# Kernel optimization log

Hardware: AMD Instinct MI355X
Metric: run time of the kernel (lower is better)

The kernel has to match this reference:

```python
import jax, jax.numpy as jnp
import numpy as np

N_NODES = 2000
LN_EPS = 1e-5
NEG_SLOPE = 0.2  # PyG GATConv default


def _gat(xg, W, b, a_src, a_dst, src, dst):
    # xg: [G, N, Fin]; single-head GATConv, add_self_loops=False
    h = xg @ W                      # [G, N, H]
    es = h @ a_src                  # [G, N]
    ed = h @ a_dst                  # [G, N]
    e = jax.nn.leaky_relu(es[:, src] + ed[:, dst], NEG_SLOPE)  # [G, E]

    def seg_softmax(e_g):
        m = jax.ops.segment_max(e_g, dst, num_segments=N_NODES)
        ex = jnp.exp(e_g - m[dst])
        s = jax.ops.segment_sum(ex, dst, num_segments=N_NODES)
        return ex / (s[dst] + 1e-16)

    alpha = jax.vmap(seg_softmax)(e)            # [G, E]
    msg = alpha[..., None] * h[:, src]          # [G, E, H]
    agg = jax.vmap(lambda m_: jax.ops.segment_sum(m_, dst, num_segments=N_NODES))(msg)
    return agg + b                              # [G, N, H]


def _gcn_layer(x, W, b, a_src, a_dst, src, dst):
    # x: [B, N, T, F] -- faithfully replicate original permute + raw reshape
    B, N, T, F = x.shape
    x_in = jnp.transpose(x, (0, 2, 1, 3)).reshape(B * T, N, F)
    out = _gat(x_in, W, b, a_src, a_dst, src, dst)          # [B*T, N, H]
    out = jax.nn.gelu(out.reshape(B, T, N, -1), approximate=False)
    # original does .reshape(B, N, T, -1) on a [B,T,N,H]-contiguous tensor
    return out.reshape(B, N, T, -1)


def _lstm(x, Wih, Whh, bih, bhh):
    # x: [BN, T, Fin]; torch LSTM gate order i,f,g,o
    BN, T, _ = x.shape
    H = Whh.shape[1]
    xz = x @ Wih.T + (bih + bhh)                # [BN, T, 4H]

    def step(carry, z_t):
        h, c = carry
        z = z_t + h @ Whh.T
        i, f, g, o = jnp.split(z, 4, axis=-1)
        c = jax.nn.sigmoid(f) * c + jax.nn.sigmoid(i) * jnp.tanh(g)
        h = jax.nn.sigmoid(o) * jnp.tanh(c)
        return (h, c), h

    init = (jnp.zeros((BN, H), x.dtype), jnp.zeros((BN, H), x.dtype))
    _, hs = jax.lax.scan(step, init, jnp.swapaxes(xz, 0, 1))
    return jnp.swapaxes(hs, 0, 1)               # [BN, T, H]


def setup_inputs() -> dict:
    key = jax.random.key(0)
    ks = jax.random.split(key, 20)
    B, N, T, NX, H, PL, NY, E = 2, N_NODES, 24, 8, 64, 12, 1, 32000
    p = {}
    p["x"] = jax.random.normal(ks[0], (B, N, T, NX), jnp.float32)
    p["edge_src"] = jax.random.randint(ks[1], (E,), 0, N, jnp.int32)
    p["edge_dst"] = jax.random.randint(ks[2], (E,), 0, N, jnp.int32)
    p["fc_W"] = jax.random.normal(ks[3], (NX, H), jnp.float32) / np.sqrt(NX)
    p["fc_b"] = jnp.zeros((H,), jnp.float32)
    for i, tag in enumerate(["g1", "g2"]):
        p[f"{tag}_W"] = jax.random.normal(ks[4 + 4 * i], (H, H), jnp.float32) / np.sqrt(H)
        p[f"{tag}_b"] = jnp.zeros((H,), jnp.float32)
        p[f"{tag}_asrc"] = jax.random.normal(ks[5 + 4 * i], (H,), jnp.float32) / np.sqrt(H)
        p[f"{tag}_adst"] = jax.random.normal(ks[6 + 4 * i], (H,), jnp.float32) / np.sqrt(H)
    p["lstm_Wih"] = jax.random.normal(ks[12], (4 * H, H), jnp.float32) / np.sqrt(H)
    p["lstm_Whh"] = jax.random.normal(ks[13], (4 * H, H), jnp.float32) / np.sqrt(H)
    p["lstm_bih"] = jnp.zeros((4 * H,), jnp.float32)
    p["lstm_bhh"] = jnp.zeros((4 * H,), jnp.float32)
    p["ln_g"] = jnp.ones((H,), jnp.float32)
    p["ln_b"] = jnp.zeros((H,), jnp.float32)
    p["dense_W"] = jax.random.normal(ks[14], (H, PL * NY), jnp.float32) / np.sqrt(H)
    p["dense_b"] = jnp.zeros((PL * NY,), jnp.float32)
    return p


def reference(x, edge_src, edge_dst, fc_W, fc_b,
              g1_W, g1_b, g1_asrc, g1_adst,
              g2_W, g2_b, g2_asrc, g2_adst,
              lstm_Wih, lstm_Whh, lstm_bih, lstm_bhh,
              ln_g, ln_b, dense_W, dense_b):
    B, N, T, _ = x.shape
    PRED_LEN, NY = 12, 1
    x_h = x @ fc_W + fc_b                                        # [B,N,T,H]
    g1 = _gcn_layer(x_h, g1_W, g1_b, g1_asrc, g1_adst, edge_src, edge_dst)
    g2 = _gcn_layer(g1, g2_W, g2_b, g2_asrc, g2_adst, edge_src, edge_dst)
    H = g2.shape[-1]
    lout = _lstm(g2.reshape(B * N, T, -1), lstm_Wih, lstm_Whh, lstm_bih, lstm_bhh)
    lout = lout.reshape(B, N, T, H)
    mu = jnp.mean(lout, axis=-1, keepdims=True)
    var = jnp.mean(jnp.square(lout - mu), axis=-1, keepdims=True)
    h = (lout - mu) / jnp.sqrt(var + LN_EPS) * ln_g + ln_b
    out = h[:, :, -1:, :] @ dense_W + dense_b                    # [B,N,1,PL*NY]
    return out.reshape(B, N, PRED_LEN, NY)
```

## Files before the change

kernel.cpp:

```cpp
#include <hip/hip_runtime.h>
#include <hip/hip_bf16.h>
#include <math.h>

#define B_   2
#define N_   2000
#define T_   24
#define NX_  8
#define H_   64
#define G_   (B_*T_)
#define E_   32000
#define BN_  (B_*N_)
#define TH_  (T_*H_)
#define NTH_ (N_*T_*H_)
#define GNH_ (G_*N_*H_)
#define NPARAM_ 43340
#define NPARAM_PAD_ 43392
#define XSTRIDE 1568
#define HPAD 96
#define DEGCAP 64

using bf16 = __hip_bfloat16;
typedef short bf16x8 __attribute__((ext_vector_type(8)));
typedef float f32x4  __attribute__((ext_vector_type(4)));

__device__ __forceinline__ float uasf(unsigned u){ return __uint_as_float(u); }
__device__ __forceinline__ float wave_sum(float v){
  #pragma unroll
  for (int o = 32; o > 0; o >>= 1) v += __shfl_xor(v, o, 64);
  return v;
}
__device__ __forceinline__ float fastrcp(float x){ return __builtin_amdgcn_rcpf(x); }
__device__ __forceinline__ float sigf(float x){ return fastrcp(1.f + __expf(-x)); }
__device__ __forceinline__ float tanhfast(float x){ return 1.f - 2.f*fastrcp(1.f + __expf(2.f*x)); }
__device__ __forceinline__ float gelu_fast(float x){
  float s = x*0.70710678118654752f;
  float a = fabsf(s);
  float t = fastrcp(1.f + 0.3275911f*a);
  float p = t*(0.254829592f + t*(-0.284496736f + t*(1.421413741f + t*(-1.453152027f + t*1.061405429f))));
  float er = 1.f - p*__expf(-a*a);
  er = (s < 0.f) ? -er : er;
  return 0.5f*x*(1.f + er);
}
__device__ __forceinline__ unsigned f2bf_rtn(float f){
  unsigned u = __float_as_uint(f);
  u += 0x7fffu + ((u >> 16) & 1u);
  return u >> 16;
}
__device__ __forceinline__ bf16x8 pack8(float4 a, float4 b){
  bf16x8 v;
  v[0]=(short)f2bf_rtn(a.x); v[1]=(short)f2bf_rtn(a.y);
  v[2]=(short)f2bf_rtn(a.z); v[3]=(short)f2bf_rtn(a.w);
  v[4]=(short)f2bf_rtn(b.x); v[5]=(short)f2bf_rtn(b.y);
  v[6]=(short)f2bf_rtn(b.z); v[7]=(short)f2bf_rtn(b.w);
  return v;
}

struct ConvArgs {
  const void* src[18];
  int off[19];
};
__global__ __launch_bounds__(256) void prep_kernel(
    ConvArgs a, const unsigned* __restrict__ xw,
    float* __restrict__ dst, int* __restrict__ flag,
    int* __restrict__ cnt_g,
    float* __restrict__ wc, float* __restrict__ bc){
  __shared__ int scnt;
  int tid = threadIdx.x;
  if (tid == 0) scnt = 0;
  __syncthreads();
  int c = 0;
  for (int i = tid; i < 4096; i += 256){
    unsigned e = (xw[i] >> 7) & 0xffu;
    if (e >= 100u && e <= 140u) c++;
  }
  atomicAdd(&scnt, c);
  __syncthreads();
  int isbf = (scnt > 3276) ? 1 : 0;
  int bid = blockIdx.x;

  if (bid < 170){
    if (bid == 0 && tid == 0) *flag = isbf;
    int i = bid*256 + tid;
    if (i < NPARAM_){
      int seg = 0;
      while (i >= a.off[seg+1]) seg++;
      int j = i - a.off[seg];
      float v;
      if (isbf) v = uasf(((unsigned)((const unsigned short*)a.src[seg])[j]) << 16);
      else      v = ((const float*)a.src[seg])[j];
      dst[i] = v;
    }
  } else if (bid == 170){
    for (int i = tid; i < N_; i += 256) cnt_g[i] = 0;
  } else if (bid < 180){
    int lane = tid & 63, wave = tid >> 6;
    int b = bid - 171;
    const unsigned short* fcWu = (const unsigned short*)a.src[0];
    const unsigned short* fcbu = (const unsigned short*)a.src[1];
    const unsigned short* g1Wu = (const unsigned short*)a.src[2];
    const float* fcWf = (const float*)a.src[0];
    const float* fcbf = (const float*)a.src[1];
    const float* g1Wf = (const float*)a.src[2];
    #pragma unroll
    for (int s = 0; s < 16; ++s){
      int o = b*64 + wave*16 + s;
      int r = o >> 6;
      int n = o & 63;
      float fa, fb;
      if (isbf){
        fa = (r < 8) ? uasf(((unsigned)fcWu[r*64 + lane]) << 16)
                     : uasf(((unsigned)fcbu[lane]) << 16);
        fb = uasf(((unsigned)g1Wu[lane*64 + n]) << 16);
      } else {
        fa = (r < 8) ? fcWf[r*64 + lane] : fcbf[lane];
        fb = g1Wf[lane*64 + n];
      }
      float sv = wave_sum(fa * fb);
      if (lane == 0){
        if (r < 8) wc[r*64 + n] = sv;
        else       bc[n] = sv;
      }
    }
  } else {
    int lane = tid & 63, wave = tid >> 6;
    int isA = (bid == 180);
    const unsigned short* g2Wu = (const unsigned short*)a.src[6];
    const float* g2Wf = (const float*)a.src[6];
    const unsigned short* au = (const unsigned short*)a.src[isA ? 8 : 9];
    const float* af = (const float*)a.src[isA ? 8 : 9];
    float fb = isbf ? uasf(((unsigned)au[lane]) << 16) : af[lane];
    #pragma unroll
    for (int s = 0; s < 16; ++s){
      int k = wave*16 + s;
      float fa = isbf ? uasf(((unsigned)g2Wu[k*64 + lane]) << 16)
                      : uasf(f2bf_rtn(g2Wf[k*64 + lane]) << 16);
      float sv = wave_sum(fa * fb);
      if (lane == 0) wc[(isA ? 576 : 640) + k] = sv;
    }
  }
}

__global__ __launch_bounds__(256) void gat_h1_fused_kernel(
    const void* __restrict__ xraw, const int* __restrict__ flag,
    const int* __restrict__ esrc, const int* __restrict__ edst,
    int* __restrict__ cnt_g, int* __restrict__ slot,
    const float* __restrict__ wc, const float* __restrict__ bc,
    const float* __restrict__ asrc, const float* __restrict__ adst,
    unsigned short* __restrict__ hbuf, float* __restrict__ es, float* __restrict__ ed){
  if (blockIdx.x < 125){
    int e = blockIdx.x*256 + threadIdx.x;
    int d = edst[e];
    int pos = atomicAdd(&cnt_g[d], 1);
    if (pos < DEGCAP) slot[(d << 6) + pos] = esrc[e];
  }
  int lane = threadIdx.x & 63, wave = threadIdx.x >> 6;
  int q = lane >> 4, c = lane & 15;
  int isbf = *flag;
  bf16x8 Bf[4];
  #pragma unroll
  for (int nt = 0; nt < 4; ++nt){
    bf16x8 v;
    #pragma unroll
    for (int j = 0; j < 8; ++j)
      v[j] = (q == 0) ? (short)f2bf_rtn(wc[j*64 + nt*16 + c]) : (short)0;
    Bf[nt] = v;
  }
  float bcv[4];
  #pragma unroll
  for (int nt = 0; nt < 4; ++nt) bcv[nt] = bc[nt*16 + c];
  float aS[4], aD[4];
  #pragma unroll
  for (int nt = 0; nt < 4; ++nt){ aS[nt] = asrc[nt*16+c]; aD[nt] = adst[nt*16+c]; }

  int w = blockIdx.x*4 + wave;
  #pragma unroll
  for (int it = 0; it < 2; ++it){
    int tile = w*2 + it;
    int p0 = tile*16;
    int g  = p0 / N_, n0 = p0 - g*N_;
    int bb = g / T_,  tt = g - bb*T_;
    bf16x8 A0;
    #pragma unroll
    for (int j = 0; j < 8; ++j) A0[j] = 0;
    if (q == 0){
      size_t rowelt = ((size_t)(bb*N_ + n0 + c)*T_ + tt)*NX_;
      if (isbf){
        A0 = *(const bf16x8*)((const unsigned short*)xraw + rowelt);
      } else {
        const float4* xr4 = (const float4*)((const float*)xraw + rowelt);
        A0 = pack8(xr4[0], xr4[1]);
      }
    }
    f32x4 acc[4];
    #pragma unroll
    for (int nt = 0; nt < 4; ++nt){ acc[nt][0]=bcv[nt]; acc[nt][1]=bcv[nt]; acc[nt][2]=bcv[nt]; acc[nt][3]=bcv[nt]; }
    #pragma unroll
    for (int nt = 0; nt < 4; ++nt) acc[nt] = __builtin_amdgcn_mfma_f32_16x16x32_bf16(A0, Bf[nt], acc[nt], 0, 0, 0);

    #pragma unroll
    for (int nt = 0; nt < 4; ++nt){
      #pragma unroll
      for (int r = 0; r < 4; ++r)
        hbuf[(size_t)(p0 + q*4 + r)*H_ + nt*16 + c] = (unsigned short)f2bf_rtn(acc[nt][r]);
    }
    #pragma unroll
    for (int r = 0; r < 4; ++r){
      float e1 = acc[0][r]*aS[0] + acc[1][r]*aS[1] + acc[2][r]*aS[2] + acc[3][r]*aS[3];
      float e2 = acc[0][r]*aD[0] + acc[1][r]*aD[1] + acc[2][r]*aD[2] + acc[3][r]*aD[3];
      #pragma unroll
      for (int o = 8; o > 0; o >>= 1){
        e1 += __shfl_xor(e1, o, 64);
        e2 += __shfl_xor(e2, o, 64);
      }
      if (c == 0){
        es[p0 + q*4 + r] = e1;
        ed[p0 + q*4 + r] = e2;
      }
    }
  }
}

__global__ __launch_bounds__(256) void gat_agg1_kernel(
    const unsigned short* __restrict__ hbuf, const float* __restrict__ es, const float* __restrict__ ed,
    const int* __restrict__ cnt_g, const int* __restrict__ slot,
    const float* __restrict__ bias, unsigned short* __restrict__ goutb,
    const float* __restrict__ wa2, const float* __restrict__ wd2,
    float* __restrict__ es2, float* __restrict__ ed2){
  int lane = threadIdx.x & 63, wave = threadIdx.x >> 6;
  int qd = lane >> 4, ln = lane & 15;
  int gd = (blockIdx.x*4 + wave)*4 + qd;
  int g = gd / N_, d = gd - g*N_;
  int start = d << 6;
  int deg = min(cnt_g[d], DEGCAP);
  const float* esg = es + (size_t)g*N_;
  float edv = ed[(size_t)g*N_ + d];
  const char* hg = (const char*)(hbuf + (size_t)g*N_*H_);
  unsigned lanoff = ((unsigned)ln) << 3;
  int hbase = qd << 4;
  int dm = deg;
  dm = max(dm, __shfl_xor(dm, 16, 64));
  dm = max(dm, __shfl_xor(dm, 32, 64));
  int NC = (dm + 15) >> 4;

  int svk[4];
  #pragma unroll
  for (int k = 0; k < 4; ++k) svk[k] = 0;
  #pragma unroll
  for (int k = 0; k < 4; ++k){
    int i = k*16 + ln;
    if (k < NC && i < deg) svk[k] = slot[start + i];
  }
  float exk[4]; float ssum = 0.f;
  #pragma unroll
  for (int k = 0; k < 4; ++k){
    int i = k*16 + ln;
    float e = 0.f;
    if (k < NC && i < deg){
      float v = esg[svk[k]] + edv;
      v = v > 0.f ? v : 0.2f*v;
      e = __expf(fminf(v, 60.f));
    }
    exk[k] = e; ssum += e;
  }
  #pragma unroll
  for (int o = 8; o > 0; o >>= 1) ssum += __shfl_xor(ssum, o, 64);
  float inv = fastrcp(ssum + 1e-16f);
  unsigned pwk[4];
  #pragma unroll
  for (int k = 0; k < 4; ++k)
    pwk[k] = (f2bf_rtn(exk[k]*inv) << 16) | (unsigned)svk[k];

  float a0 = 0.f, a1 = 0.f, a2 = 0.f, a3 = 0.f;
  for (int k = 0; k < NC; ++k){
    unsigned pw = pwk[k];
    int myrem = deg - k*16;
    int remw = dm - k*16; if (remw > 16) remw = 16;
    for (int j0 = 0; j0 < remw; j0 += 8){
      unsigned wv[8]; float aa[8]; unsigned off[8];
      #pragma unroll
      for (int u = 0; u < 8; ++u){
        int j = j0 + u;
        wv[u] = (unsigned)__shfl((int)pw, hbase + j, 64);
        aa[u] = (j < myrem) ? uasf(wv[u] & 0xffff0000u) : 0.f;
        off[u] = ((wv[u] & 0xffffu) << 7) + lanoff;
      }
      uint2 hv[8];
      #pragma unroll
      for (int u = 0; u < 8; ++u)
        hv[u] = *(const uint2*)(hg + off[u]);
      #pragma unroll
      for (int u = 0; u < 8; ++u){
        a0 = fmaf(aa[u], uasf(hv[u].x << 16), a0);
        a1 = fmaf(aa[u], uasf(hv[u].x & 0xffff0000u), a1);
        a2 = fmaf(aa[u], uasf(hv[u].y << 16), a2);
        a3 = fmaf(aa[u], uasf(hv[u].y & 0xffff0000u), a3);
      }
    }
  }
  float4 bv = ((const float4*)bias)[ln];
  float g0 = gelu_fast(a0 + bv.x), g1 = gelu_fast(a1 + bv.y);
  float g2v = gelu_fast(a2 + bv.z), g3 = gelu_fast(a3 + bv.w);
  uint2 ov;
  ov.x = f2bf_rtn(g0) | (f2bf_rtn(g1) << 16);
  ov.y = f2bf_rtn(g2v) | (f2bf_rtn(g3) << 16);
  ((uint2*)(goutb + (size_t)gd*H_))[ln] = ov;

  float h0 = uasf(ov.x << 16), h1v = uasf(ov.x & 0xffff0000u);
  float h2v = uasf(ov.y << 16), h3v = uasf(ov.y & 0xffff0000u);
  f32x4 wa = *(const f32x4*)(wa2 + ln*4);
  f32x4 wd = *(const f32x4*)(wd2 + ln*4);
  float e1 = h0*wa[0] + h1v*wa[1] + h2v*wa[2] + h3v*wa[3];
  float e2 = h0*wd[0] + h1v*wd[1] + h2v*wd[2] + h3v*wd[3];
  #pragma unroll
  for (int o = 8; o > 0; o >>= 1){
    e1 += __shfl_xor(e1, o, 64);
    e2 += __shfl_xor(e2, o, 64);
  }
  if (ln == 0){
    int bbp = gd / (N_*T_);
    int rem = gd - bbp*(N_*T_);
    int np  = rem / T_;
    int tp  = rem - np*T_;
    int pprime = (bbp*T_ + tp)*N_ + np;
    es2[pprime] = e1;
    ed2[pprime] = e2;
  }
}

__global__ __launch_bounds__(256) void gat_agg2_kernel(
    const unsigned short* __restrict__ goutb, const float* __restrict__ es, const float* __restrict__ ed,
    const int* __restrict__ cnt_g, const int* __restrict__ slot,
    const float* __restrict__ W, const float* __restrict__ b2,
    unsigned short* __restrict__ outb){
  __shared__ __align__(16) float vlds[4*256];
  int lane = threadIdx.x & 63, wave = threadIdx.x >> 6;
  int qd = lane >> 4, ln = lane & 15;
  int gd = (blockIdx.x*4 + wave)*4 + qd;
  int g = gd / N_, d = gd - g*N_;
  int bb2 = g / T_, t2 = g - bb2*T_;
  int start = d << 6;
  int deg = min(cnt_g[d], DEGCAP);
  const float* esg = es + (size_t)g*N_;
  float edv = ed[(size_t)g*N_ + d];
  const char* hgb = (const char*)goutb + (size_t)bb2*(size_t)(NTH_*2) + (size_t)t2*128 + (((unsigned)ln) << 3);
  int hbase = qd << 4;
  int dm = deg;
  dm = max(dm, __shfl_xor(dm, 16, 64));
  dm = max(dm, __shfl_xor(dm, 32, 64));
  int NC = (dm + 15) >> 4;

  bf16x8 Bf[4][2];
  #pragma unroll
  for (int nt = 0; nt < 4; ++nt){
    #pragma unroll
    for (int ks = 0; ks < 2; ++ks){
      bf16x8 v;
      #pragma unroll
      for (int j = 0; j < 8; ++j)
        v[j] = (short)f2bf_rtn(W[(ks*32 + qd*8 + j)*H_ + nt*16 + ln]);
      Bf[nt][ks] = v;
    }
  }
  float bcv[4];
  #pragma unroll
  for (int nt = 0; nt < 4; ++nt) bcv[nt] = b2[nt*16 + ln];

  int svk[4];
  #pragma unroll
  for (int k = 0; k < 4; ++k) svk[k] = 0;
  #pragma unroll
  for (int k = 0; k < 4; ++k){
    int i = k*16 + ln;
    if (k < NC && i < deg) svk[k] = slot[start + i];
  }
  float exk[4]; float ssum = 0.f;
  #pragma unroll
  for (int k = 0; k < 4; ++k){
    int i = k*16 + ln;
    float e = 0.f;
    if (k < NC && i < deg){
      float v = esg[svk[k]] + edv;
      v = v > 0.f ? v : 0.2f*v;
      e = __expf(fminf(v, 60.f));
    }
    exk[k] = e; ssum += e;
  }
  #pragma unroll
  for (int o = 8; o > 0; o >>= 1) ssum += __shfl_xor(ssum, o, 64);
  float inv = fastrcp(ssum + 1e-16f);
  unsigned pwk[4];
  #pragma unroll
  for (int k = 0; k < 4; ++k)
    pwk[k] = (f2bf_rtn(exk[k]*inv) << 16) | (unsigned)svk[k];

  float a0 = 0.f, a1 = 0.f, a2 = 0.f, a3 = 0.f;
  for (int k = 0; k < NC; ++k){
    unsigned pw = pwk[k];
    int myrem = deg - k*16;
    int remw = dm - k*16; if (remw > 16) remw = 16;
    for (int j0 = 0; j0 < remw; j0 += 8){
      unsigned wv[8]; float aa[8]; unsigned off[8];
      #pragma unroll
      for (int u = 0; u < 8; ++u){
        int j = j0 + u;
        wv[u] = (unsigned)__shfl((int)pw, hbase + j, 64);
        aa[u] = (j < myrem) ? uasf(wv[u] & 0xffff0000u) : 0.f;
        off[u] = (wv[u] & 0xffffu) * 3072u;
      }
      uint2 hv[8];
      #pragma unroll
      for (int u = 0; u < 8; ++u)
        hv[u] = *(const uint2*)(hgb + off[u]);
      #pragma unroll
      for (int u = 0; u < 8; ++u){
        a0 = fmaf(aa[u], uasf(hv[u].x << 16), a0);
        a1 = fmaf(aa[u], uasf(hv[u].x & 0xffff0000u), a1);
        a2 = fmaf(aa[u], uasf(hv[u].y << 16), a2);
        a3 = fmaf(aa[u], uasf(hv[u].y & 0xffff0000u), a3);
      }
    }
  }

  unsigned short* vu = (unsigned short*)vlds + wave*512;
  uint2 vp;
  vp.x = f2bf_rtn(a0) | (f2bf_rtn(a1) << 16);
  vp.y = f2bf_rtn(a2) | (f2bf_rtn(a3) << 16);
  *(uint2*)(vu + qd*64 + ln*4) = vp;
  bf16x8 Af0 = *(const bf16x8*)(vu + (ln & 3)*64 + qd*8);
  bf16x8 Af1 = *(const bf16x8*)(vu + (ln & 3)*64 + 32 + qd*8);

  f32x4 acc[4];
  #pragma unroll
  for (int nt = 0; nt < 4; ++nt){ acc[nt][0]=0.f; acc[nt][1]=0.f; acc[nt][2]=0.f; acc[nt][3]=0.f; }
  #pragma unroll
  for (int nt = 0; nt < 4; ++nt) acc[nt] = __builtin_amdgcn_mfma_f32_16x16x32_bf16(Af0, Bf[nt][0], acc[nt], 0, 0, 0);
  #pragma unroll
  for (int nt = 0; nt < 4; ++nt) acc[nt] = __builtin_amdgcn_mfma_f32_16x16x32_bf16(Af1, Bf[nt][1], acc[nt], 0, 0, 0);

  float* vf = vlds + wave*256;
  if (qd == 0){
    #pragma unroll
    for (int nt = 0; nt < 4; ++nt){
      #pragma unroll
      for (int r = 0; r < 4; ++r)
        vf[r*64 + nt*16 + ln] = acc[nt][r] + bcv[nt];
    }
  }
  __syncthreads();
  f32x4 vo = *(const f32x4*)(vf + qd*64 + ln*4);
  uint2 ov;
  ov.x = f2bf_rtn(gelu_fast(vo[0])) | (f2bf_rtn(gelu_fast(vo[1])) << 16);
  ov.y = f2bf_rtn(gelu_fast(vo[2])) | (f2bf_rtn(gelu_fast(vo[3])) << 16);
  ((uint2*)(outb + (size_t)gd*H_))[ln] = ov;
}

__global__ __launch_bounds__(256) void lstm_final_kernel(
    const unsigned short* __restrict__ xinb,
    const float* __restrict__ Wih,
    const float* __restrict__ Whh,
    const float* __restrict__ bih, const float* __restrict__ bhh,
    const float* __restrict__ lng, const float* __restrict__ lnb,
    const float* __restrict__ dW, const float* __restrict__ db,
    const int* __restrict__ flag, void* __restrict__ outv){
  __shared__ __align__(16) unsigned short Xlds[4*XSTRIDE];
  __shared__ __align__(16) unsigned short Hlds[2][4*HPAD];
  __shared__ float smH[4][68];
  int tid = threadIdx.x;
  int lane = tid & 63, wave = tid >> 6;
  int q = lane >> 4, c = lane & 15;
  int cc = c >> 2;
  int s0 = blockIdx.x * 4;

  {
    const unsigned short* xg = xinb + (size_t)s0 * TH_;
    #pragma unroll
    for (int ch0 = 0; ch0 < 12; ch0 += 4){
      int ch = ch0 + wave;
      int r = ch / 3, jj = ch - r*3;
      bf16x8 v = *(const bf16x8*)(xg + r*1536 + jj*512 + lane*8);
      *(bf16x8*)(Xlds + r*XSTRIDE + jj*512 + lane*8) = v;
    }
  }

  bf16x8 Bf[4][4];
  #pragma unroll
  for (int g = 0; g < 4; ++g){
    int n = g*64 + wave*16 + c;
    #pragma unroll
    for (int ks = 0; ks < 4; ++ks){
      const float* srcp = (ks < 2) ? (Whh + (size_t)n*64 + ks*32 + q*8)
                                   : (Wih + (size_t)n*64 + (ks-2)*32 + q*8);
      float4 a = ((const float4*)srcp)[0];
      float4 b = ((const float4*)srcp)[1];
      Bf[g][ks] = pack8(a, b);
    }
  }
  float bsum[4];
  #pragma unroll
  for (int g = 0; g < 4; ++g){
    int n = g*64 + wave*16 + c;
    bsum[g] = bih[n] + bhh[n];
  }
  for (int i = tid; i < 4*HPAD; i += 256) Hlds[0][i] = 0;
  float cst = 0.f;
  __syncthreads();

  const unsigned short* xrow = Xlds + cc*XSTRIDE;
  bf16x8 Ax0 = *(const bf16x8*)(xrow + q*8);
  bf16x8 Ax1 = *(const bf16x8*)(xrow + 32 + q*8);

  int buf = 0;
  for (int t = 0; t < T_; ++t){
    bf16x8 Ah0 = *(const bf16x8*)(Hlds[buf] + cc*HPAD + q*8);
    bf16x8 Ah1 = *(const bf16x8*)(Hlds[buf] + cc*HPAD + 32 + q*8);

    f32x4 acc[4];
    #pragma unroll
    for (int g = 0; g < 4; ++g){ acc[g][0]=bsum[g]; acc[g][1]=bsum[g]; acc[g][2]=bsum[g]; acc[g][3]=bsum[g]; }
    #pragma unroll
    for (int g = 0; g < 4; ++g) acc[g] = __builtin_amdgcn_mfma_f32_16x16x32_bf16(Ax0, Bf[g][2], acc[g], 0, 0, 0);
    #pragma unroll
    for (int g = 0; g < 4; ++g) acc[g] = __builtin_amdgcn_mfma_f32_16x16x32_bf16(Ax1, Bf[g][3], acc[g], 0, 0, 0);
    #pragma unroll
    for (int g = 0; g < 4; ++g) acc[g] = __builtin_amdgcn_mfma_f32_16x16x32_bf16(Ah0, Bf[g][0], acc[g], 0, 0, 0);
    #pragma unroll
    for (int g = 0; g < 4; ++g) acc[g] = __builtin_amdgcn_mfma_f32_16x16x32_bf16(Ah1, Bf[g][1], acc[g], 0, 0, 0);

    int tn = (t < T_-1) ? t+1 : T_-1;
    bf16x8 AxN0 = *(const bf16x8*)(xrow + tn*64 + q*8);
    bf16x8 AxN1 = *(const bf16x8*)(xrow + tn*64 + 32 + q*8);

    float zi = acc[0][0], zf = acc[1][0], zg = acc[2][0], zo = acc[3][0];
    cst = sigf(zf)*cst + sigf(zi)*tanhfast(zg);
    float hv = sigf(zo)*tanhfast(cst);

    if (t == T_-1){
      smH[q][wave*16 + c] = hv;
    } else {
      Hlds[buf^1][q*HPAD + wave*16 + c] = (unsigned short)f2bf_rtn(hv);
      __syncthreads();
      buf ^= 1;
    }
    Ax0 = AxN0; Ax1 = AxN1;
  }
  __syncthreads();

  int isbf = *flag;
  {
    int s = wave;
    float h = smH[s][lane];
    float mu = wave_sum(h) * (1.f/64.f);
    float dev = h - mu;
    float var = wave_sum(dev*dev) * (1.f/64.f);
    float hn = dev * rsqrtf(var + 1e-5f) * lng[lane] + lnb[lane];
    smH[s][lane] = hn;
    if (lane < 12){
      float o = db[lane];
      #pragma unroll
      for (int k = 0; k < 64; ++k) o = fmaf(smH[s][k], dW[k*12 + lane], o);
      size_t oi = (size_t)(s0 + s)*12 + lane;
      if (isbf) ((unsigned short*)outv)[oi] = (unsigned short)f2bf_rtn(o);
      else      ((float*)outv)[oi] = o;
    }
  }
}

extern "C" void kernel_launch(void* const* d_in, const int* in_sizes, int n_in,
                              void* d_out, int out_size, void* d_ws, size_t ws_size,
                              hipStream_t stream) {
  const int* esrc = (const int*)d_in[1];
  const int* edst = (const int*)d_in[2];

  static const int sizes[18] = {512, 64, 4096, 64, 64, 64, 4096, 64, 64, 64,
                                16384, 16384, 256, 256, 64, 64, 768, 12};
  static const int srcidx[18] = {3, 4, 5, 6, 7, 8, 9, 10, 11, 12,
                                 13, 14, 15, 16, 17, 18, 19, 20};
  ConvArgs ca;
  {
    int acc = 0;
    for (int i = 0; i < 18; ++i){ ca.src[i] = d_in[srcidx[i]]; ca.off[i] = acc; acc += sizes[i]; }
    ca.off[18] = acc;
  }

  float* P     = (float*)d_ws;
  float* bufA  = P + NPARAM_PAD_;
  float* bufB  = bufA + (size_t)GNH_/2 + 64;
  float* esb   = bufB + (size_t)GNH_/2 + 64;
  float* edb   = esb  + (size_t)G_*N_;
  int*   cnt_g = (int*)(edb + (size_t)G_*N_);
  int*   slot  = cnt_g + N_;
  int*   flag  = slot + N_*DEGCAP;
  float* wcb   = (float*)(flag + 1);
  float* es2b  = wcb + 704;
  float* ed2b  = es2b + (size_t)G_*N_;
  unsigned short* goutb = (unsigned short*)bufA;
  unsigned short* hbuf  = (unsigned short*)bufB;

  const float* pg1b = P + 4672;
  const float* pg1as= P + 4736;
  const float* pg1ad= P + 4800;
  const float* pg2W = P + 4864;
  const float* pg2b = P + 8960;
  const float* pWih = P + 9152;
  const float* pWhh = P + 25536;
  const float* pbih = P + 41920;
  const float* pbhh = P + 42176;
  const float* plng = P + 42432;
  const float* plnb = P + 42496;
  const float* pdW  = P + 42560;
  const float* pdb  = P + 43328;

  prep_kernel<<<182, 256, 0, stream>>>(ca, (const unsigned*)d_in[0],
                                       P, flag, cnt_g, wcb, wcb + 512);

  gat_h1_fused_kernel<<<750, 256, 0, stream>>>(d_in[0], flag, esrc, edst, cnt_g, slot,
                                               wcb, wcb + 512, pg1as, pg1ad, hbuf, esb, edb);

  gat_agg1_kernel<<<6000, 256, 0, stream>>>(hbuf, esb, edb, cnt_g, slot, pg1b, goutb,
                                            wcb + 576, wcb + 640, es2b, ed2b);

  gat_agg2_kernel<<<6000, 256, 0, stream>>>(goutb, es2b, ed2b, cnt_g, slot,
                                            pg2W, pg2b, hbuf);

  lstm_final_kernel<<<1000, 256, 0, stream>>>(hbuf, pWih, pWhh, pbih, pbhh,
                                              plng, plnb, pdW, pdb, flag, d_out);
}
```

Before: 234.2 us.

## Precompute second-layer GAT projection with MFMA before gather-aggregation

```diff
diff --git a/kernel.cpp b/kernel.cpp
--- a/kernel.cpp
+++ b/kernel.cpp
@@ -273,15 +273,13 @@
   float a0 = 0.f, a1 = 0.f, a2 = 0.f, a3 = 0.f;
   for (int k = 0; k < NC; ++k){
     unsigned pw = pwk[k];
-    int myrem = deg - k*16;
     int remw = dm - k*16; if (remw > 16) remw = 16;
     for (int j0 = 0; j0 < remw; j0 += 8){
       unsigned wv[8]; float aa[8]; unsigned off[8];
       #pragma unroll
       for (int u = 0; u < 8; ++u){
-        int j = j0 + u;
-        wv[u] = (unsigned)__shfl((int)pw, hbase + j, 64);
-        aa[u] = (j < myrem) ? uasf(wv[u] & 0xffff0000u) : 0.f;
+        wv[u] = (unsigned)__shfl((int)pw, hbase + j0 + u, 64);
+        aa[u] = uasf(wv[u] & 0xffff0000u);
         off[u] = ((wv[u] & 0xffffu) << 7) + lanoff;
       }
       uint2 hv[8];
@@ -298,11 +296,9 @@
     }
   }
   float4 bv = ((const float4*)bias)[ln];
-  float g0 = gelu_fast(a0 + bv.x), g1 = gelu_fast(a1 + bv.y);
-  float g2v = gelu_fast(a2 + bv.z), g3 = gelu_fast(a3 + bv.w);
   uint2 ov;
-  ov.x = f2bf_rtn(g0) | (f2bf_rtn(g1) << 16);
-  ov.y = f2bf_rtn(g2v) | (f2bf_rtn(g3) << 16);
+  ov.x = f2bf_rtn(gelu_fast(a0 + bv.x)) | (f2bf_rtn(gelu_fast(a1 + bv.y)) << 16);
+  ov.y = f2bf_rtn(gelu_fast(a2 + bv.z)) | (f2bf_rtn(gelu_fast(a3 + bv.w)) << 16);
   ((uint2*)(goutb + (size_t)gd*H_))[ln] = ov;
 
   float h0 = uasf(ov.x << 16), h1v = uasf(ov.x & 0xffff0000u);
@@ -327,43 +323,72 @@
   }
 }
 
+__global__ __launch_bounds__(256) void gat_h2_mfma_kernel(
+    const unsigned short* __restrict__ xinb, const float* __restrict__ W,
+    unsigned short* __restrict__ hbuf){
+  int lane = threadIdx.x & 63, wave = threadIdx.x >> 6;
+  int q = lane >> 4, c = lane & 15;
+  bf16x8 Bf[4][2];
+  #pragma unroll
+  for (int nt = 0; nt < 4; ++nt){
+    #pragma unroll
+    for (int ks = 0; ks < 2; ++ks){
+      bf16x8 v;
+      #pragma unroll
+      for (int j = 0; j < 8; ++j)
+        v[j] = (short)f2bf_rtn(W[(ks*32 + q*8 + j)*H_ + nt*16 + c]);
+      Bf[nt][ks] = v;
+    }
+  }
+
+  int w = blockIdx.x*4 + wave;
+  #pragma unroll
+  for (int it = 0; it < 2; ++it){
+    int tile = w*2 + it;
+    int p0 = tile*16;
+    int p  = p0 + c;
+    int g = p / N_, n = p - g*N_;
+    int bb = g / T_, t = g - bb*T_;
+    const unsigned short* xr = xinb + (size_t)bb*NTH_ + (size_t)n*TH_ + (size_t)t*H_;
+    bf16x8 A0 = *(const bf16x8*)(xr + q*8);
+    bf16x8 A1 = *(const bf16x8*)(xr + 32 + q*8);
+
+    f32x4 acc[4];
+    #pragma unroll
+    for (int nt = 0; nt < 4; ++nt){ acc[nt][0]=0.f; acc[nt][1]=0.f; acc[nt][2]=0.f; acc[nt][3]=0.f; }
+    #pragma unroll
+    for (int nt = 0; nt < 4; ++nt) acc[nt] = __builtin_amdgcn_mfma_f32_16x16x32_bf16(A0, Bf[nt][0], acc[nt], 0, 0, 0);
+    #pragma unroll
+    for (int nt = 0; nt < 4; ++nt) acc[nt] = __builtin_amdgcn_mfma_f32_16x16x32_bf16(A1, Bf[nt][1], acc[nt], 0, 0, 0);
+
+    #pragma unroll
+    for (int nt = 0; nt < 4; ++nt){
+      #pragma unroll
+      for (int r = 0; r < 4; ++r)
+        hbuf[(size_t)(p0 + q*4 + r)*H_ + nt*16 + c] = (unsigned short)f2bf_rtn(acc[nt][r]);
+    }
+  }
+}
+
 __global__ __launch_bounds__(256) void gat_agg2_kernel(
-    const unsigned short* __restrict__ goutb, const float* __restrict__ es, const float* __restrict__ ed,
+    const unsigned short* __restrict__ hbuf, const float* __restrict__ es, const float* __restrict__ ed,
     const int* __restrict__ cnt_g, const int* __restrict__ slot,
-    const float* __restrict__ W, const float* __restrict__ b2,
-    unsigned short* __restrict__ outb){
-  __shared__ __align__(16) float vlds[4*256];
+    const float* __restrict__ bias, unsigned short* __restrict__ goutb){
   int lane = threadIdx.x & 63, wave = threadIdx.x >> 6;
   int qd = lane >> 4, ln = lane & 15;
   int gd = (blockIdx.x*4 + wave)*4 + qd;
   int g = gd / N_, d = gd - g*N_;
-  int bb2 = g / T_, t2 = g - bb2*T_;
   int start = d << 6;
   int deg = min(cnt_g[d], DEGCAP);
   const float* esg = es + (size_t)g*N_;
   float edv = ed[(size_t)g*N_ + d];
-  const char* hgb = (const char*)goutb + (size_t)bb2*(size_t)(NTH_*2) + (size_t)t2*128 + (((unsigned)ln) << 3);
+  const char* hg = (const char*)(hbuf + (size_t)g*N_*H_);
+  unsigned lanoff = ((unsigned)ln) << 3;
   int hbase = qd << 4;
   int dm = deg;
   dm = max(dm, __shfl_xor(dm, 16, 64));
   dm = max(dm, __shfl_xor(dm, 32, 64));
   int NC = (dm + 15) >> 4;
-
-  bf16x8 Bf[4][2];
-  #pragma unroll
-  for (int nt = 0; nt < 4; ++nt){
-    #pragma unroll
-    for (int ks = 0; ks < 2; ++ks){
-      bf16x8 v;
-      #pragma unroll
-      for (int j = 0; j < 8; ++j)
-        v[j] = (short)f2bf_rtn(W[(ks*32 + qd*8 + j)*H_ + nt*16 + ln]);
-      Bf[nt][ks] = v;
-    }
-  }
-  float bcv[4];
-  #pragma unroll
-  for (int nt = 0; nt < 4; ++nt) bcv[nt] = b2[nt*16 + ln];
 
   int svk[4];
   #pragma unroll
@@ -396,21 +421,19 @@
   float a0 = 0.f, a1 = 0.f, a2 = 0.f, a3 = 0.f;
   for (int k = 0; k < NC; ++k){
     unsigned pw = pwk[k];
-    int myrem = deg - k*16;
     int remw = dm - k*16; if (remw > 16) remw = 16;
     for (int j0 = 0; j0 < remw; j0 += 8){
       unsigned wv[8]; float aa[8]; unsigned off[8];
       #pragma unroll
       for (int u = 0; u < 8; ++u){
-        int j = j0 + u;
-        wv[u] = (unsigned)__shfl((int)pw, hbase + j, 64);
-        aa[u] = (j < myrem) ? uasf(wv[u] & 0xffff0000u) : 0.f;
-        off[u] = (wv[u] & 0xffffu) * 3072u;
+        wv[u] = (unsigned)__shfl((int)pw, hbase + j0 + u, 64);
+        aa[u] = uasf(wv[u] & 0xffff0000u);
+        off[u] = ((wv[u] & 0xffffu) << 7) + lanoff;
       }
       uint2 hv[8];
       #pragma unroll
       for (int u = 0; u < 8; ++u)
-        hv[u] = *(const uint2*)(hgb + off[u]);
+        hv[u] = *(const uint2*)(hg + off[u]);
       #pragma unroll
       for (int u = 0; u < 8; ++u){
         a0 = fmaf(aa[u], uasf(hv[u].x << 16), a0);
@@ -420,38 +443,11 @@
       }
     }
   }
-
-  unsigned short* vu = (unsigned short*)vlds + wave*512;
-  uint2 vp;
-  vp.x = f2bf_rtn(a0) | (f2bf_rtn(a1) << 16);
-  vp.y = f2bf_rtn(a2) | (f2bf_rtn(a3) << 16);
-  *(uint2*)(vu + qd*64 + ln*4) = vp;
-  bf16x8 Af0 = *(const bf16x8*)(vu + (ln & 3)*64 + qd*8);
-  bf16x8 Af1 = *(const bf16x8*)(vu + (ln & 3)*64 + 32 + qd*8);
-
-  f32x4 acc[4];
-  #pragma unroll
-  for (int nt = 0; nt < 4; ++nt){ acc[nt][0]=0.f; acc[nt][1]=0.f; acc[nt][2]=0.f; acc[nt][3]=0.f; }
-  #pragma unroll
-  for (int nt = 0; nt < 4; ++nt) acc[nt] = __builtin_amdgcn_mfma_f32_16x16x32_bf16(Af0, Bf[nt][0], acc[nt], 0, 0, 0);
-  #pragma unroll
-  for (int nt = 0; nt < 4; ++nt) acc[nt] = __builtin_amdgcn_mfma_f32_16x16x32_bf16(Af1, Bf[nt][1], acc[nt], 0, 0, 0);
-
-  float* vf = vlds + wave*256;
-  if (qd == 0){
-    #pragma unroll
-    for (int nt = 0; nt < 4; ++nt){
-      #pragma unroll
-      for (int r = 0; r < 4; ++r)
-        vf[r*64 + nt*16 + ln] = acc[nt][r] + bcv[nt];
-    }
-  }
-  __syncthreads();
-  f32x4 vo = *(const f32x4*)(vf + qd*64 + ln*4);
+  float4 bv = ((const float4*)bias)[ln];
   uint2 ov;
-  ov.x = f2bf_rtn(gelu_fast(vo[0])) | (f2bf_rtn(gelu_fast(vo[1])) << 16);
-  ov.y = f2bf_rtn(gelu_fast(vo[2])) | (f2bf_rtn(gelu_fast(vo[3])) << 16);
-  ((uint2*)(outb + (size_t)gd*H_))[ln] = ov;
+  ov.x = f2bf_rtn(gelu_fast(a0 + bv.x)) | (f2bf_rtn(gelu_fast(a1 + bv.y)) << 16);
+  ov.y = f2bf_rtn(gelu_fast(a2 + bv.z)) | (f2bf_rtn(gelu_fast(a3 + bv.w)) << 16);
+  ((uint2*)(goutb + (size_t)gd*H_))[ln] = ov;
 }
 
 __global__ __launch_bounds__(256) void lstm_final_kernel(
@@ -619,9 +615,10 @@
   gat_agg1_kernel<<<6000, 256, 0, stream>>>(hbuf, esb, edb, cnt_g, slot, pg1b, goutb,
                                             wcb + 576, wcb + 640, es2b, ed2b);
 
-  gat_agg2_kernel<<<6000, 256, 0, stream>>>(goutb, es2b, ed2b, cnt_g, slot,
-                                            pg2W, pg2b, hbuf);
-
-  lstm_final_kernel<<<1000, 256, 0, stream>>>(hbuf, pWih, pWhh, pbih, pbhh,
+  gat_h2_mfma_kernel<<<750, 256, 0, stream>>>(goutb, pg2W, hbuf);
+
+  gat_agg2_kernel<<<6000, 256, 0, stream>>>(hbuf, es2b, ed2b, cnt_g, slot, pg2b, goutb);
+
+  lstm_final_kernel<<<1000, 256, 0, stream>>>(goutb, pWih, pWhh, pbih, pbhh,
                                               plng, plnb, pdW, pdb, flag, d_out);
 }
```

New measurement: 228.5 us. 2.4% less time.
